# Kernel optimization log

Measured on AMD Instinct MI355X. Metric: run time of the kernel, lower is better.

## Reference

```python
import jax, jax.numpy as jnp
import numpy as np

N, IN_F, OUT_F, K = 256, 8192, 8320, 16
J = OUT_F - IN_F  # 128


def setup_inputs() -> dict:
    key = jax.random.key(0)
    k1, k2 = jax.random.split(key)
    tensor = jax.random.normal(k1, (N, IN_F), dtype=jnp.float32)
    T = jax.random.normal(k2, (IN_F, J, K), dtype=jnp.float32)
    return {"tensor": tensor, "T": T}


def reference(tensor, T):
    # flatten(start_dim=1) is identity for rank-2 input
    x = tensor.reshape(tensor.shape[0], -1)            # [N, IN_F]
    feats = jnp.einsum('ni,ijk->njk', x, T)            # [N, J, K]
    # pairwise L1 across batch: [N,1,J,K] - [N,J,K] -> [N,N,J,K]
    diff = jnp.abs(feats[:, None, :, :] - feats[None, :, :, :])
    l1 = jnp.sum(diff, axis=3)                         # [N, N, J]
    diversity = jnp.sum(jnp.exp(-l1), axis=1)          # [N, J]
    return jnp.concatenate((x, diversity), axis=1)     # [N, IN_F + J]
```

## Files before the change

### kernel.cpp

```cpp
#include <hip/hip_runtime.h>

typedef unsigned int  u32;
typedef unsigned short u16;

typedef __bf16 bf16x8 __attribute__((ext_vector_type(8)));
typedef u32    u32x4  __attribute__((ext_vector_type(4)));
typedef float  floatx4 __attribute__((ext_vector_type(4)));

#define N_ROWS 256
#define IN_F   8192
#define OUT_F  8320
#define JDIM   128
#define KDIM   16
#define JK     2048

#define BN      64
#define KSLAB   512
#define NSLAB   16

__device__ __forceinline__ u16 f2bf(float f) {
    u32 u = __float_as_uint(f);
    return (u16)((u + 0x7fffu + ((u >> 16) & 1u)) >> 16);
}
__device__ __forceinline__ float bf2f(u16 h) { return __uint_as_float(((u32)h) << 16); }

__global__ __launch_bounds__(256) void prep_kernel(const float* __restrict__ X,
                                                   float* __restrict__ out,
                                                   u16* __restrict__ Xb)
{
    int t = blockIdx.x * 256 + threadIdx.x;
    float4 v = reinterpret_cast<const float4*>(X)[t];
    int row = t >> 11;
    int c4  = t & 2047;
    reinterpret_cast<float4*>(out + (size_t)row * OUT_F)[c4] = v;
    ushort4 b;
    b.x = f2bf(v.x); b.y = f2bf(v.y); b.z = f2bf(v.z); b.w = f2bf(v.w);
    reinterpret_cast<ushort4*>(Xb)[t] = b;
    if (t < 8192) {
        int r2 = t >> 5, j4 = t & 31;
        reinterpret_cast<float4*>(out + (size_t)r2 * OUT_F + IN_F)[j4] = make_float4(0.f, 0.f, 0.f, 0.f);
    }
}

__global__ __launch_bounds__(256) void gemm_kernel(const u16* __restrict__ Xb,
                                                   const float* __restrict__ W,
                                                   u16* __restrict__ slabs)
{
    const int tid  = threadIdx.x;
    const int lane = tid & 63;
    const int wave = tid >> 6;
    const int c0   = blockIdx.x * BN;
    const int s    = blockIdx.y;
    const int k0   = s * KSLAB;

    const int h  = wave >> 1;
    const int cc = wave & 1;
    const int n  = lane & 15;
    const int q  = lane >> 4;

    floatx4 acc[8][2] = {};

    const u32* wbase = (const u32*)W + (size_t)(k0 + q * 8) * JK + c0 + cc * 32 + n;
    const u16* abase = Xb + k0 + q * 8;

    u32 ub[2][8], ubn[2][8];
    bf16x8 a[8], an[8];

    #pragma unroll
    for (int cbi = 0; cbi < 2; ++cbi)
        #pragma unroll
        for (int j = 0; j < 8; ++j)
            ub[cbi][j] = wbase[(size_t)j * JK + cbi * 16];
    #pragma unroll
    for (int rf = 0; rf < 8; ++rf)
        a[rf] = *(const bf16x8*)(abase + (size_t)(h * 128 + rf * 16 + n) * IN_F);

    const int KC = KSLAB / 32;
    for (int kc = 0; kc < KC; ++kc) {
        if (kc + 1 < KC) {
            const u32* wp = wbase + (size_t)(kc + 1) * 32 * JK;
            #pragma unroll
            for (int cbi = 0; cbi < 2; ++cbi)
                #pragma unroll
                for (int j = 0; j < 8; ++j)
                    ubn[cbi][j] = wp[(size_t)j * JK + cbi * 16];
            #pragma unroll
            for (int rf = 0; rf < 8; ++rf)
                an[rf] = *(const bf16x8*)(abase + (size_t)(h * 128 + rf * 16 + n) * IN_F + (kc + 1) * 32);
        }

        bf16x8 b[2];
        #pragma unroll
        for (int cbi = 0; cbi < 2; ++cbi) {
            u32x4 pk;
            #pragma unroll
            for (int t = 0; t < 4; ++t)
                pk[t] = (ub[cbi][2 * t] >> 16) | (ub[cbi][2 * t + 1] & 0xffff0000u);
            b[cbi] = __builtin_bit_cast(bf16x8, pk);
        }

        #pragma unroll
        for (int rf = 0; rf < 8; ++rf)
            #pragma unroll
            for (int cbi = 0; cbi < 2; ++cbi)
                acc[rf][cbi] = __builtin_amdgcn_mfma_f32_16x16x32_bf16(a[rf], b[cbi], acc[rf][cbi], 0, 0, 0);

        #pragma unroll
        for (int cbi = 0; cbi < 2; ++cbi)
            #pragma unroll
            for (int j = 0; j < 8; ++j)
                ub[cbi][j] = ubn[cbi][j];
        #pragma unroll
        for (int rf = 0; rf < 8; ++rf)
            a[rf] = an[rf];
    }

    u16* sp = slabs + (size_t)s * N_ROWS * JK;
    #pragma unroll
    for (int rf = 0; rf < 8; ++rf)
        #pragma unroll
        for (int cbi = 0; cbi < 2; ++cbi)
            #pragma unroll
            for (int r = 0; r < 4; ++r) {
                int row = h * 128 + rf * 16 + q * 4 + r;
                int col = c0 + cc * 32 + cbi * 16 + n;
                sp[(size_t)row * JK + col] = f2bf(acc[rf][cbi][r]);
            }
}

__global__ __launch_bounds__(256) void reduce_kernel(const u16* __restrict__ slabs,
                                                     float* __restrict__ feats)
{
    int t = blockIdx.x * 256 + threadIdx.x;
    float acc[8] = {};
    for (int s = 0; s < NSLAB; ++s) {
        uint4 v = *(const uint4*)(slabs + (size_t)s * N_ROWS * JK + (size_t)t * 8);
        const u16* h = (const u16*)&v;
        #pragma unroll
        for (int e = 0; e < 8; ++e) acc[e] += bf2f(h[e]);
    }
    float4* fp = (float4*)(feats + (size_t)t * 8);
    fp[0] = make_float4(acc[0], acc[1], acc[2], acc[3]);
    fp[1] = make_float4(acc[4], acc[5], acc[6], acc[7]);
}

__global__ __launch_bounds__(256) void pairwise_kernel(const float* __restrict__ feats,
                                                       float* __restrict__ out)
{
    const int j = blockIdx.x;
    const int mq = blockIdx.y;
    const int n = threadIdx.x;

    __shared__ float F[N_ROWS * KDIM];
    const float* fr = feats + (size_t)n * JK + j * KDIM;
    float4 v0 = ((const float4*)fr)[0];
    float4 v1 = ((const float4*)fr)[1];
    float4 v2 = ((const float4*)fr)[2];
    float4 v3 = ((const float4*)fr)[3];
    float4* Fp = (float4*)&F[n * KDIM];
    Fp[0] = v0; Fp[1] = v1; Fp[2] = v2; Fp[3] = v3;
    __syncthreads();

    float f[16] = { v0.x, v0.y, v0.z, v0.w, v1.x, v1.y, v1.z, v1.w,
                    v2.x, v2.y, v2.z, v2.w, v3.x, v3.y, v3.z, v3.w };
    float accum = 0.f;
    const int m0 = mq * 64;
    for (int m = 0; m < 64; ++m) {
        const float* Fm = &F[(m0 + m) * KDIM];
        float l1 = 0.f;
        #pragma unroll
        for (int k = 0; k < 16; ++k) l1 += fabsf(f[k] - Fm[k]);
        accum += exp2f(-1.4426950408889634f * l1);
    }
    atomicAdd(&out[(size_t)n * OUT_F + IN_F + j], accum);
}

extern "C" void kernel_launch(void* const* d_in, const int* in_sizes, int n_in,
                              void* d_out, int out_size, void* d_ws, size_t ws_size,
                              hipStream_t stream)
{
    const float* X = (const float*)d_in[0];
    const float* T = (const float*)d_in[1];
    float* out = (float*)d_out;

    float* feats = (float*)d_ws;
    u16*   Xb    = (u16*)((char*)d_ws + (2u << 20));
    u16*   slabs = (u16*)((char*)d_ws + (6u << 20));

    prep_kernel<<<2048, 256, 0, stream>>>(X, out, Xb);
    gemm_kernel<<<dim3(JK / BN, NSLAB), 256, 0, stream>>>(Xb, T, slabs);
    reduce_kernel<<<256, 256, 0, stream>>>(slabs, feats);
    pairwise_kernel<<<dim3(JDIM, 4), 256, 0, stream>>>(feats, out);
}
```

Before: 158.7 us.

## Stage bf16-packed weight tiles in shared memory with 512-thread GEMM blocks

```diff
diff --git a/kernel.cpp b/kernel.cpp
--- a/kernel.cpp
+++ b/kernel.cpp
@@ -14,9 +14,10 @@
 #define KDIM   16
 #define JK     2048
 
-#define BN      64
-#define KSLAB   512
-#define NSLAB   16
+#define BN     256
+#define BKC    32
+#define NSLAB  32
+#define PC     257
 
 __device__ __forceinline__ u16 f2bf(float f) {
     u32 u = __float_as_uint(f);
@@ -42,89 +43,108 @@
     }
 }
 
-__global__ __launch_bounds__(256) void gemm_kernel(const u16* __restrict__ Xb,
+__global__ __launch_bounds__(512) void gemm_kernel(const u16* __restrict__ Xb,
                                                    const float* __restrict__ W,
                                                    u16* __restrict__ slabs)
 {
+    __shared__ u32 wt[2 * 16 * PC];
+
     const int tid  = threadIdx.x;
     const int lane = tid & 63;
-    const int wave = tid >> 6;
+    const int w    = tid >> 6;
     const int c0   = blockIdx.x * BN;
     const int s    = blockIdx.y;
-    const int k0   = s * KSLAB;
-
-    const int h  = wave >> 1;
-    const int cc = wave & 1;
+    const int k0   = s * (IN_F / NSLAB);
+
     const int n  = lane & 15;
     const int q  = lane >> 4;
-
-    floatx4 acc[8][2] = {};
-
-    const u32* wbase = (const u32*)W + (size_t)(k0 + q * 8) * JK + c0 + cc * 32 + n;
+    const int rp = tid >> 5;
+    const int u  = tid & 31;
+
+    const int wr0 = (w & 3) * 64;
+    const int wc0 = (w >> 2) * 128;
+
+    floatx4 acc[4][8] = {};
+
+    const float* wbase = W + (size_t)(k0 + 2 * rp) * JK + c0 + 4 * u;
+
+    float4 wreg[4];
+    wreg[0] = *(const float4*)(wbase);
+    wreg[1] = *(const float4*)(wbase + 128);
+    wreg[2] = *(const float4*)(wbase + (size_t)JK);
+    wreg[3] = *(const float4*)(wbase + (size_t)JK + 128);
+
     const u16* abase = Xb + k0 + q * 8;
-
-    u32 ub[2][8], ubn[2][8];
-    bf16x8 a[8], an[8];
-
+    bf16x8 a[4], an[4];
     #pragma unroll
-    for (int cbi = 0; cbi < 2; ++cbi)
-        #pragma unroll
-        for (int j = 0; j < 8; ++j)
-            ub[cbi][j] = wbase[(size_t)j * JK + cbi * 16];
+    for (int rf = 0; rf < 4; ++rf)
+        a[rf] = *(const bf16x8*)(abase + (size_t)(wr0 + rf * 16 + n) * IN_F);
+
     #pragma unroll
-    for (int rf = 0; rf < 8; ++rf)
-        a[rf] = *(const bf16x8*)(abase + (size_t)(h * 128 + rf * 16 + n) * IN_F);
-
-    const int KC = KSLAB / 32;
-    for (int kc = 0; kc < KC; ++kc) {
-        if (kc + 1 < KC) {
-            const u32* wp = wbase + (size_t)(kc + 1) * 32 * JK;
-            #pragma unroll
-            for (int cbi = 0; cbi < 2; ++cbi)
+    for (int j = 0; j < 2; ++j)
+        #pragma unroll
+        for (int i = 0; i < 4; ++i) {
+            float lo = ((const float*)&wreg[j])[i];
+            float hi = ((const float*)&wreg[2 + j])[i];
+            wt[rp * PC + 4 * u + 128 * j + i] = (u32)f2bf(lo) | ((u32)f2bf(hi) << 16);
+        }
+    __syncthreads();
+
+    const int NCH = (IN_F / NSLAB) / BKC;
+    float4 wnx[4];
+    for (int kw = 0; kw < NCH; ++kw) {
+        const u32* buf = wt + (kw & 1) * (16 * PC);
+
+        if (kw + 1 < NCH) {
+            const float* wb2 = wbase + (size_t)(kw + 1) * BKC * JK;
+            wnx[0] = *(const float4*)(wb2);
+            wnx[1] = *(const float4*)(wb2 + 128);
+            wnx[2] = *(const float4*)(wb2 + (size_t)JK);
+            wnx[3] = *(const float4*)(wb2 + (size_t)JK + 128);
+            #pragma unroll
+            for (int rf = 0; rf < 4; ++rf)
+                an[rf] = *(const bf16x8*)(abase + (size_t)(wr0 + rf * 16 + n) * IN_F + (kw + 1) * BKC);
+        }
+
+        #pragma unroll
+        for (int cf = 0; cf < 8; ++cf) {
+            int c = wc0 + cf * 16 + n;
+            u32x4 bv;
+            #pragma unroll
+            for (int i = 0; i < 4; ++i)
+                bv[i] = buf[(q * 4 + i) * PC + c];
+            bf16x8 bfrag = __builtin_bit_cast(bf16x8, bv);
+            #pragma unroll
+            for (int rf = 0; rf < 4; ++rf)
+                acc[rf][cf] = __builtin_amdgcn_mfma_f32_16x16x32_bf16(a[rf], bfrag, acc[rf][cf], 0, 0, 0);
+        }
+
+        if (kw + 1 < NCH) {
+            u32* dbuf = wt + ((kw + 1) & 1) * (16 * PC);
+            #pragma unroll
+            for (int j = 0; j < 2; ++j)
                 #pragma unroll
-                for (int j = 0; j < 8; ++j)
-                    ubn[cbi][j] = wp[(size_t)j * JK + cbi * 16];
-            #pragma unroll
-            for (int rf = 0; rf < 8; ++rf)
-                an[rf] = *(const bf16x8*)(abase + (size_t)(h * 128 + rf * 16 + n) * IN_F + (kc + 1) * 32);
-        }
-
-        bf16x8 b[2];
-        #pragma unroll
-        for (int cbi = 0; cbi < 2; ++cbi) {
-            u32x4 pk;
-            #pragma unroll
-            for (int t = 0; t < 4; ++t)
-                pk[t] = (ub[cbi][2 * t] >> 16) | (ub[cbi][2 * t + 1] & 0xffff0000u);
-            b[cbi] = __builtin_bit_cast(bf16x8, pk);
-        }
-
-        #pragma unroll
-        for (int rf = 0; rf < 8; ++rf)
-            #pragma unroll
-            for (int cbi = 0; cbi < 2; ++cbi)
-                acc[rf][cbi] = __builtin_amdgcn_mfma_f32_16x16x32_bf16(a[rf], b[cbi], acc[rf][cbi], 0, 0, 0);
-
-        #pragma unroll
-        for (int cbi = 0; cbi < 2; ++cbi)
-            #pragma unroll
-            for (int j = 0; j < 8; ++j)
-                ub[cbi][j] = ubn[cbi][j];
-        #pragma unroll
-        for (int rf = 0; rf < 8; ++rf)
-            a[rf] = an[rf];
+                for (int i = 0; i < 4; ++i) {
+                    float lo = ((const float*)&wnx[j])[i];
+                    float hi = ((const float*)&wnx[2 + j])[i];
+                    dbuf[rp * PC + 4 * u + 128 * j + i] = (u32)f2bf(lo) | ((u32)f2bf(hi) << 16);
+                }
+            #pragma unroll
+            for (int rf = 0; rf < 4; ++rf) a[rf] = an[rf];
+            __syncthreads();
+        }
     }
 
     u16* sp = slabs + (size_t)s * N_ROWS * JK;
     #pragma unroll
-    for (int rf = 0; rf < 8; ++rf)
-        #pragma unroll
-        for (int cbi = 0; cbi < 2; ++cbi)
-            #pragma unroll
-            for (int r = 0; r < 4; ++r) {
-                int row = h * 128 + rf * 16 + q * 4 + r;
-                int col = c0 + cc * 32 + cbi * 16 + n;
-                sp[(size_t)row * JK + col] = f2bf(acc[rf][cbi][r]);
+    for (int rf = 0; rf < 4; ++rf)
+        #pragma unroll
+        for (int cf = 0; cf < 8; ++cf)
+            #pragma unroll
+            for (int rr = 0; rr < 4; ++rr) {
+                int row = wr0 + rf * 16 + q * 4 + rr;
+                int col = c0 + wc0 + cf * 16 + n;
+                sp[(size_t)row * JK + col] = f2bf(acc[rf][cf][rr]);
             }
 }
 
@@ -188,7 +208,7 @@
     u16*   slabs = (u16*)((char*)d_ws + (6u << 20));
 
     prep_kernel<<<2048, 256, 0, stream>>>(X, out, Xb);
-    gemm_kernel<<<dim3(JK / BN, NSLAB), 256, 0, stream>>>(Xb, T, slabs);
+    gemm_kernel<<<dim3(JK / BN, NSLAB), 512, 0, stream>>>(Xb, T, slabs);
     reduce_kernel<<<256, 256, 0, stream>>>(slabs, feats);
     pairwise_kernel<<<dim3(JDIM, 4), 256, 0, stream>>>(feats, out);
 }
```

New measurement: 151.6 us. -4.5%, faster.

## Pre-transpose weights to bf16 K-major and retile GEMM over rows

Applied to the files above, without the earlier changes.

```diff
diff --git a/kernel.cpp b/kernel.cpp
--- a/kernel.cpp
+++ b/kernel.cpp
@@ -4,7 +4,6 @@
 typedef unsigned short u16;
 
 typedef __bf16 bf16x8 __attribute__((ext_vector_type(8)));
-typedef u32    u32x4  __attribute__((ext_vector_type(4)));
 typedef float  floatx4 __attribute__((ext_vector_type(4)));
 
 #define N_ROWS 256
@@ -14,9 +13,11 @@
 #define KDIM   16
 #define JK     2048
 
-#define BN      64
-#define KSLAB   512
-#define NSLAB   16
+#define NSLAB  16
+#define GKSL   512
+#define TC     512
+#define TK     64
+#define LP     264
 
 __device__ __forceinline__ u16 f2bf(float f) {
     u32 u = __float_as_uint(f);
@@ -42,89 +43,108 @@
     }
 }
 
+__global__ __launch_bounds__(256) void transpose_kernel(const float* __restrict__ T,
+                                                        u16* __restrict__ Tbt)
+{
+    __shared__ u32 L[TK * LP];
+
+    const int t  = threadIdx.x;
+    const int c0 = blockIdx.x * TC;
+    const int k0 = blockIdx.y * TK;
+
+    const int c4 = t & 127;
+    const int rh = t >> 7;
+
+    #pragma unroll
+    for (int i = 0; i < 32; ++i) {
+        int r = rh * 32 + i;
+        float4 v = *(const float4*)(T + (size_t)(k0 + r) * JK + c0 + c4 * 4);
+        uint2 pk;
+        pk.x = (u32)f2bf(v.x) | ((u32)f2bf(v.y) << 16);
+        pk.y = (u32)f2bf(v.z) | ((u32)f2bf(v.w) << 16);
+        *(uint2*)&L[r * LP + c4 * 2] = pk;
+    }
+    __syncthreads();
+
+    u32 oe[32], oo[32];
+    #pragma unroll
+    for (int kp = 0; kp < 32; ++kp) {
+        u32 a = L[(2 * kp) * LP + t];
+        u32 b = L[(2 * kp + 1) * LP + t];
+        oe[kp] = (a & 0xffffu) | (b << 16);
+        oo[kp] = (a >> 16) | (b & 0xffff0000u);
+    }
+    u16* o0 = Tbt + (size_t)(c0 + 2 * t) * IN_F + k0;
+    u16* o1 = o0 + IN_F;
+    #pragma unroll
+    for (int j = 0; j < 8; ++j) {
+        *(uint4*)(o0 + j * 8) = *(uint4*)&oe[j * 4];
+        *(uint4*)(o1 + j * 8) = *(uint4*)&oo[j * 4];
+    }
+}
+
 __global__ __launch_bounds__(256) void gemm_kernel(const u16* __restrict__ Xb,
-                                                   const float* __restrict__ W,
+                                                   const u16* __restrict__ Tbt,
                                                    u16* __restrict__ slabs)
 {
     const int tid  = threadIdx.x;
     const int lane = tid & 63;
-    const int wave = tid >> 6;
-    const int c0   = blockIdx.x * BN;
-    const int s    = blockIdx.y;
-    const int k0   = s * KSLAB;
-
-    const int h  = wave >> 1;
-    const int cc = wave & 1;
-    const int n  = lane & 15;
-    const int q  = lane >> 4;
-
-    floatx4 acc[8][2] = {};
-
-    const u32* wbase = (const u32*)W + (size_t)(k0 + q * 8) * JK + c0 + cc * 32 + n;
-    const u16* abase = Xb + k0 + q * 8;
-
-    u32 ub[2][8], ubn[2][8];
-    bf16x8 a[8], an[8];
-
-    #pragma unroll
-    for (int cbi = 0; cbi < 2; ++cbi)
-        #pragma unroll
-        for (int j = 0; j < 8; ++j)
-            ub[cbi][j] = wbase[(size_t)j * JK + cbi * 16];
-    #pragma unroll
-    for (int rf = 0; rf < 8; ++rf)
-        a[rf] = *(const bf16x8*)(abase + (size_t)(h * 128 + rf * 16 + n) * IN_F);
-
-    const int KC = KSLAB / 32;
+    const int w    = tid >> 6;
+    const int c0   = blockIdx.x * 64;
+    const int m0   = blockIdx.y * 128;
+    const int s    = blockIdx.z;
+    const int k0   = s * GKSL;
+
+    const int n = lane & 15, q = lane >> 4;
+    const int wr0 = m0 + (w & 1) * 64;
+    const int wc0 = c0 + (w >> 1) * 32;
+
+    floatx4 acc[4][2] = {};
+
+    const u16* arow[4];
+    const u16* brow[2];
+    #pragma unroll
+    for (int rf = 0; rf < 4; ++rf)
+        arow[rf] = Xb + (size_t)(wr0 + rf * 16 + n) * IN_F + k0 + q * 8;
+    #pragma unroll
+    for (int cf = 0; cf < 2; ++cf)
+        brow[cf] = Tbt + (size_t)(wc0 + cf * 16 + n) * IN_F + k0 + q * 8;
+
+    bf16x8 a[4], b[2], an[4], bn[2];
+    #pragma unroll
+    for (int rf = 0; rf < 4; ++rf) a[rf] = *(const bf16x8*)(arow[rf]);
+    #pragma unroll
+    for (int cf = 0; cf < 2; ++cf) b[cf] = *(const bf16x8*)(brow[cf]);
+
+    const int KC = GKSL / 32;
     for (int kc = 0; kc < KC; ++kc) {
         if (kc + 1 < KC) {
-            const u32* wp = wbase + (size_t)(kc + 1) * 32 * JK;
-            #pragma unroll
-            for (int cbi = 0; cbi < 2; ++cbi)
-                #pragma unroll
-                for (int j = 0; j < 8; ++j)
-                    ubn[cbi][j] = wp[(size_t)j * JK + cbi * 16];
-            #pragma unroll
-            for (int rf = 0; rf < 8; ++rf)
-                an[rf] = *(const bf16x8*)(abase + (size_t)(h * 128 + rf * 16 + n) * IN_F + (kc + 1) * 32);
+            #pragma unroll
+            for (int rf = 0; rf < 4; ++rf) an[rf] = *(const bf16x8*)(arow[rf] + (kc + 1) * 32);
+            #pragma unroll
+            for (int cf = 0; cf < 2; ++cf) bn[cf] = *(const bf16x8*)(brow[cf] + (kc + 1) * 32);
         }
-
-        bf16x8 b[2];
-        #pragma unroll
-        for (int cbi = 0; cbi < 2; ++cbi) {
-            u32x4 pk;
-            #pragma unroll
-            for (int t = 0; t < 4; ++t)
-                pk[t] = (ub[cbi][2 * t] >> 16) | (ub[cbi][2 * t + 1] & 0xffff0000u);
-            b[cbi] = __builtin_bit_cast(bf16x8, pk);
-        }
-
-        #pragma unroll
-        for (int rf = 0; rf < 8; ++rf)
-            #pragma unroll
-            for (int cbi = 0; cbi < 2; ++cbi)
-                acc[rf][cbi] = __builtin_amdgcn_mfma_f32_16x16x32_bf16(a[rf], b[cbi], acc[rf][cbi], 0, 0, 0);
-
-        #pragma unroll
-        for (int cbi = 0; cbi < 2; ++cbi)
-            #pragma unroll
-            for (int j = 0; j < 8; ++j)
-                ub[cbi][j] = ubn[cbi][j];
-        #pragma unroll
-        for (int rf = 0; rf < 8; ++rf)
-            a[rf] = an[rf];
+        #pragma unroll
+        for (int rf = 0; rf < 4; ++rf)
+            #pragma unroll
+            for (int cf = 0; cf < 2; ++cf)
+                acc[rf][cf] = __builtin_amdgcn_mfma_f32_16x16x32_bf16(a[rf], b[cf], acc[rf][cf], 0, 0, 0);
+        #pragma unroll
+        for (int rf = 0; rf < 4; ++rf) a[rf] = an[rf];
+        #pragma unroll
+        for (int cf = 0; cf < 2; ++cf) b[cf] = bn[cf];
     }
 
     u16* sp = slabs + (size_t)s * N_ROWS * JK;
     #pragma unroll
-    for (int rf = 0; rf < 8; ++rf)
-        #pragma unroll
-        for (int cbi = 0; cbi < 2; ++cbi)
-            #pragma unroll
-            for (int r = 0; r < 4; ++r) {
-                int row = h * 128 + rf * 16 + q * 4 + r;
-                int col = c0 + cc * 32 + cbi * 16 + n;
-                sp[(size_t)row * JK + col] = f2bf(acc[rf][cbi][r]);
+    for (int rf = 0; rf < 4; ++rf)
+        #pragma unroll
+        for (int cf = 0; cf < 2; ++cf)
+            #pragma unroll
+            for (int rr = 0; rr < 4; ++rr) {
+                int row = wr0 + rf * 16 + q * 4 + rr;
+                int col = wc0 + cf * 16 + n;
+                sp[(size_t)row * JK + col] = f2bf(acc[rf][cf][rr]);
             }
 }
 
@@ -186,9 +206,11 @@
     float* feats = (float*)d_ws;
     u16*   Xb    = (u16*)((char*)d_ws + (2u << 20));
     u16*   slabs = (u16*)((char*)d_ws + (6u << 20));
+    u16*   Tbt   = (u16*)((char*)d_ws + (22u << 20));
 
     prep_kernel<<<2048, 256, 0, stream>>>(X, out, Xb);
-    gemm_kernel<<<dim3(JK / BN, NSLAB), 256, 0, stream>>>(Xb, T, slabs);
+    transpose_kernel<<<dim3(JK / TC, IN_F / TK), 256, 0, stream>>>(T, Tbt);
+    gemm_kernel<<<dim3(JK / 64, N_ROWS / 128, NSLAB), 256, 0, stream>>>(Xb, Tbt, slabs);
     reduce_kernel<<<256, 256, 0, stream>>>(slabs, feats);
     pairwise_kernel<<<dim3(JDIM, 4), 256, 0, stream>>>(feats, out);
 }
```

After: 184.7 us. 16.4% more time.
